# Optimization experiments

Hardware: AMD Instinct MI355X
Metric: run time of the kernel (lower is better)

The kernel has to match this reference:

```python
import jax, jax.numpy as jnp
import numpy as np

B, T, F, E, H = 1024, 128, 32, 16, 20
EPS = 1e-3  # keras BatchNormalization default epsilon
D = T * F   # flatten dim; fc1 builds with units = T*F due to pre-build units mutation


def lstm_relu(x, Wk, Wr, b, return_seq):
    """Keras LSTM with activation='relu', recurrent_activation=sigmoid.
    Gate order i, f, c(g), o. x: [B,T,Fin]. Returns [B,T,H] or [B,H]."""
    Bn = x.shape[0]
    h0 = jnp.zeros((Bn, H), x.dtype)
    c0 = jnp.zeros((Bn, H), x.dtype)

    def step(carry, xt):
        h, c = carry
        z = xt @ Wk + h @ Wr + b                      # [B, 4H]
        i, f, g, o = jnp.split(z, 4, axis=-1)
        i = jax.nn.sigmoid(i)
        f = jax.nn.sigmoid(f)
        g = jax.nn.relu(g)
        o = jax.nn.sigmoid(o)
        c = f * c + i * g
        h = o * jax.nn.relu(c)
        return (h, c), h

    (hT, _), hs = jax.lax.scan(step, (h0, c0), jnp.swapaxes(x, 0, 1))
    return jnp.swapaxes(hs, 0, 1) if return_seq else hT


def setup_inputs():
    key = jax.random.key(0)
    ks = jax.random.split(key, 16)
    s = 0.1
    d = {}
    d["x"] = jax.random.normal(ks[0], (B, T, F), jnp.float32)
    # BatchNorm (inference: moving stats)
    d["bn_gamma"] = jnp.ones((F,), jnp.float32)
    d["bn_beta"] = jnp.zeros((F,), jnp.float32)
    d["bn_mean"] = jax.random.normal(ks[1], (F,), jnp.float32) * 0.1
    d["bn_var"] = jax.random.uniform(ks[2], (F,), jnp.float32, 0.5, 1.5)
    # Per-expert LSTM stacks (stacked over expert axis E)
    d["k1"] = jax.random.normal(ks[3], (E, F, 4 * H), jnp.float32) * s
    d["r1"] = jax.random.normal(ks[4], (E, H, 4 * H), jnp.float32) * s
    d["b1"] = jnp.zeros((E, 4 * H), jnp.float32)
    d["k2"] = jax.random.normal(ks[5], (E, H, 4 * H), jnp.float32) * s
    d["r2"] = jax.random.normal(ks[6], (E, H, 4 * H), jnp.float32) * s
    d["b2"] = jnp.zeros((E, 4 * H), jnp.float32)
    d["dw"] = jax.random.normal(ks[7], (E, H, 1), jnp.float32) * s
    d["db"] = jnp.zeros((E, 1), jnp.float32)
    # Gating path: flatten -> Dense(D, relu) -> Dense(E, softmax)
    d["fc1_w"] = jax.random.normal(ks[8], (D, D), jnp.float32) * 0.02
    d["fc1_b"] = jnp.zeros((D,), jnp.float32)
    d["gate_w"] = jax.random.normal(ks[9], (D, E), jnp.float32) * 0.02
    d["gate_b"] = jnp.zeros((E,), jnp.float32)
    return d


def reference(x, bn_gamma, bn_beta, bn_mean, bn_var,
              k1, r1, b1, k2, r2, b2, dw, db,
              fc1_w, fc1_b, gate_w, gate_b):
    # BatchNorm (inference) over last axis
    xn = (x - bn_mean) * jax.lax.rsqrt(bn_var + EPS) * bn_gamma + bn_beta

    def run_expert(k1e, r1e, b1e, k2e, r2e, b2e, dwe, dbe):
        h1 = lstm_relu(xn, k1e, r1e, b1e, return_seq=True)    # [B,T,H]
        h2 = lstm_relu(h1, k2e, r2e, b2e, return_seq=False)   # [B,H]
        return h2 @ dwe + dbe                                  # [B,1]

    expert_outputs = jax.vmap(run_expert)(k1, r1, b1, k2, r2, b2, dw, db)  # [E,B,1]

    flat = x.reshape(x.shape[0], -1)                    # [B, T*F] (raw inputs, not normed)
    g = jax.nn.relu(flat @ fc1_w + fc1_b)               # [B, D]
    w = jax.nn.softmax(g @ gate_w + gate_b, axis=-1)    # [B, E]

    # stack(axis=1) -> [B,E,1]; weights expand_dims(axis=2) -> [B,E,1]; sum over E
    out = jnp.sum(jnp.transpose(expert_outputs, (1, 0, 2)) * w[:, :, None], axis=1)  # [B,1]
    return out
```

## Files before the change

kernel.cpp:

```cpp
#include <hip/hip_runtime.h>
#include <math.h>

#define Bsz 1024
#define Tt  128
#define Ff  32
#define Ee  16
#define Hh  20
#define Dd  4096
#define EPSc 1e-3f
#define LOG2E 1.4426950408889634f

#define PWE 7520

typedef __attribute__((ext_vector_type(8))) short bf16x8;
typedef __attribute__((ext_vector_type(4))) float f32x4;
typedef __attribute__((ext_vector_type(4))) unsigned int u32x4;

#define MFMA16(a,b,c) __builtin_amdgcn_mfma_f32_16x16x32_bf16(a, b, c, 0, 0, 0)

__device__ __forceinline__ float sig2(float z) {
    return __builtin_amdgcn_rcpf(1.0f + __builtin_amdgcn_exp2f(-z));
}
__device__ __forceinline__ unsigned short bf16_rne(float f) {
    unsigned u = __float_as_uint(f);
    u += 0x7FFFu + ((u >> 16) & 1u);
    return (unsigned short)(u >> 16);
}
__device__ __forceinline__ float bf16_to_f(unsigned short h) {
    return __uint_as_float(((unsigned)h) << 16);
}
__device__ __forceinline__ void cvt2(float f0, float f1, unsigned& hp, unsigned& lp) {
    asm("v_cvt_pk_bf16_f32 %0, %1, %2" : "=v"(hp) : "v"(f0), "v"(f1));
    float h0 = __uint_as_float(hp << 16);
    float h1 = __uint_as_float(hp & 0xFFFF0000u);
    asm("v_cvt_pk_bf16_f32 %0, %1, %2" : "=v"(lp) : "v"(f0 - h0), "v"(f1 - h1));
}

__global__ void xpack_kernel(const float* __restrict__ x,
                             const float* __restrict__ gamma, const float* __restrict__ beta,
                             const float* __restrict__ mean,  const float* __restrict__ var,
                             unsigned short* __restrict__ xph, unsigned short* __restrict__ xpl)
{
    __shared__ float sc[Ff], sh[Ff];
    int tid = threadIdx.x;
    if (tid < Ff) {
        float s = gamma[tid] * rsqrtf(var[tid] + EPSc);
        sc[tid] = s;
        sh[tid] = beta[tid] - mean[tid] * s;
    }
    __syncthreads();
    int idx = blockIdx.x * 256 + tid;
    int c   = idx >> 13;
    int rem = idx & 8191;
    int t   = rem >> 6;
    int l   = rem & 63;
    int q   = l >> 4, s = l & 15;
    const float* xr = x + ((size_t)(c * 16 + s) * Tt + t) * Ff + q * 8;
    float4 v0 = *(const float4*)xr;
    float4 v1 = *(const float4*)(xr + 4);
    float xv[8] = {v0.x, v0.y, v0.z, v0.w, v1.x, v1.y, v1.z, v1.w};
    bf16x8 hv, lv;
#pragma unroll
    for (int j = 0; j < 8; ++j) {
        int f = q * 8 + j;
        float xn_ = xv[j] * sc[f] + sh[f];
        unsigned short hi = bf16_rne(xn_);
        hv[j] = (short)hi;
        lv[j] = (short)bf16_rne(xn_ - bf16_to_f(hi));
    }
    *(bf16x8*)(xph + (size_t)idx * 8) = hv;
    *(bf16x8*)(xpl + (size_t)idx * 8) = lv;
}

__global__ void repack2_kernel(const float* __restrict__ k1, const float* __restrict__ r1,
                               const float* __restrict__ b1, const float* __restrict__ k2,
                               const float* __restrict__ r2, const float* __restrict__ b2,
                               float* __restrict__ pw)
{
    int idx = blockIdx.x * blockDim.x + threadIdx.x;
    if (idx >= Ee * PWE) return;
    int e = idx / PWE;
    int o = idx % PWE;
    float v;
    int g;
    if (o < 7360) {
        int c = o % 80, u = c >> 2;
        g = c & 3;
        int co = g * 20 + u;
        if (o < 2560) {
            int kk = o / 80;
            v = k1[((size_t)e * Ff + kk) * 80 + co];
        } else if (o < 4160) {
            int kk = (o - 2560) / 80;
            v = r1[((size_t)e * Hh + kk) * 80 + co];
        } else if (o < 5760) {
            int kk = (o - 4160) / 80;
            v = k2[((size_t)e * Hh + kk) * 80 + co];
        } else {
            int kk = (o - 5760) / 80;
            v = r2[((size_t)e * Hh + kk) * 80 + co];
        }
    } else if (o < 7440) {
        int c = o - 7360, u = c >> 2;
        g = c & 3;
        v = b1[(size_t)e * 80 + g * 20 + u];
    } else {
        int c = o - 7440, u = c >> 2;
        g = c & 3;
        v = b2[(size_t)e * 80 + g * 20 + u];
    }
    if (g != 2) v *= LOG2E;
    pw[idx] = v;
}

__global__ __launch_bounds__(256, 2) void fused_kernel(
    const unsigned short* __restrict__ xph, const unsigned short* __restrict__ xpl,
    const float* __restrict__ pw, const float* __restrict__ dw, const float* __restrict__ db,
    float* __restrict__ eo,
    const float* __restrict__ x, const float* __restrict__ W,
    const float* __restrict__ bias, float* __restrict__ C)
{
    __shared__ __align__(16) char smem[43008];

    if (blockIdx.x < 256) {
        const int l = threadIdx.x & 63;
        const int q = l >> 4, s = l & 15;
        const int tile = (blockIdx.x << 2) + (threadIdx.x >> 6);
        const int e = tile >> 6;
        const int c = tile & 63;
        const int b0 = c * 16;

        const float* Wm = pw + (size_t)e * PWE;
        bf16x8 K1h[5], K1l[5], R1h[5], R1l[5], K2h[5], K2l[5], R2h[5], R2l[5];
#pragma unroll
        for (int n = 0; n < 5; ++n) {
#pragma unroll
            for (int j = 0; j < 8; ++j) {
                int k8 = q * 8 + j;
                int uk = 4 * j + q;
                int cc = n * 16 + s;
                float wv_;
                unsigned short hi; float hf;
                wv_ = Wm[k8 * 80 + cc];
                hi = bf16_rne(wv_); hf = bf16_to_f(hi);
                K1h[n][j] = (short)hi; K1l[n][j] = (short)bf16_rne(wv_ - hf);
                wv_ = (j < 5) ? Wm[2560 + uk * 80 + cc] : 0.f;
                hi = bf16_rne(wv_); hf = bf16_to_f(hi);
                R1h[n][j] = (short)hi; R1l[n][j] = (short)bf16_rne(wv_ - hf);
                wv_ = (j < 5) ? Wm[4160 + uk * 80 + cc] : 0.f;
                hi = bf16_rne(wv_); hf = bf16_to_f(hi);
                K2h[n][j] = (short)hi; K2l[n][j] = (short)bf16_rne(wv_ - hf);
                wv_ = (j < 5) ? Wm[5760 + uk * 80 + cc] : 0.f;
                hi = bf16_rne(wv_); hf = bf16_to_f(hi);
                R2h[n][j] = (short)hi; R2l[n][j] = (short)bf16_rne(wv_ - hf);
            }
        }
        f32x4 bf1[5], bf2[5];
        float dwr[5];
#pragma unroll
        for (int n = 0; n < 5; ++n) {
            bf1[n] = *(const f32x4*)&Wm[7360 + n * 16 + 4 * q];
            bf2[n] = *(const f32x4*)&Wm[7440 + n * 16 + 4 * q];
            dwr[n] = dw[e * Hh + 4 * n + q];
        }

        float c1[5] = {0, 0, 0, 0, 0}, c2[5] = {0, 0, 0, 0, 0};
        float h2reg[5] = {0, 0, 0, 0, 0};

        const bf16x8 z8 = {0, 0, 0, 0, 0, 0, 0, 0};
        bf16x8 H1a = z8, H1b = z8, H2a = z8, H2b = z8;

        const unsigned short* xbh = xph + (size_t)c * 65536 + l * 8;
        const unsigned short* xbl = xpl + (size_t)c * 65536 + l * 8;
        bf16x8 xch = *(const bf16x8*)xbh;
        bf16x8 xcl = *(const bf16x8*)xbl;

#pragma unroll 1
        for (int t = 0; t < Tt; ++t) {
            bf16x8 xnh = xch, xnl = xcl;
            if (t < Tt - 1) {
                xnh = *(const bf16x8*)(xbh + (t + 1) * 512);
                xnl = *(const bf16x8*)(xbl + (t + 1) * 512);
            }

            f32x4 a1[5];
#pragma unroll
            for (int n = 0; n < 5; ++n) {
                f32x4 acc = bf1[n];
                acc = MFMA16(K1h[n], xch, acc);
                acc = MFMA16(K1l[n], xch, acc);
                acc = MFMA16(K1h[n], xcl, acc);
                acc = MFMA16(R1h[n], H1a, acc);
                acc = MFMA16(R1l[n], H1a, acc);
                acc = MFMA16(R1h[n], H1b, acc);
                a1[n] = acc;
            }
            {
                float hv[5];
#pragma unroll
                for (int n = 0; n < 5; ++n) {
                    float iv = sig2(a1[n][0]);
                    float fv = sig2(a1[n][1]);
                    float gv = fmaxf(a1[n][2], 0.f);
                    float ov = sig2(a1[n][3]);
                    c1[n] = fv * c1[n] + iv * gv;
                    hv[n] = ov * fmaxf(c1[n], 0.f);
                }
                unsigned h0, h1, h2, l0, l1, l2;
                cvt2(hv[0], hv[1], h0, l0);
                cvt2(hv[2], hv[3], h1, l1);
                cvt2(hv[4], 0.f,   h2, l2);
                u32x4 uh = {h0, h1, h2, 0u}, ul = {l0, l1, l2, 0u};
                H1a = __builtin_bit_cast(bf16x8, uh);
                H1b = __builtin_bit_cast(bf16x8, ul);
            }

            f32x4 a2[5];
#pragma unroll
            for (int n = 0; n < 5; ++n) {
                f32x4 acc = bf2[n];
                acc = MFMA16(R2h[n], H2a, acc);
                acc = MFMA16(R2l[n], H2a, acc);
                acc = MFMA16(R2h[n], H2b, acc);
                acc = MFMA16(K2h[n], H1a, acc);
                acc = MFMA16(K2l[n], H1a, acc);
                acc = MFMA16(K2h[n], H1b, acc);
                a2[n] = acc;
            }
            {
                float hv[5];
#pragma unroll
                for (int n = 0; n < 5; ++n) {
                    float iv = sig2(a2[n][0]);
                    float fv = sig2(a2[n][1]);
                    float gv = fmaxf(a2[n][2], 0.f);
                    float ov = sig2(a2[n][3]);
                    c2[n] = fv * c2[n] + iv * gv;
                    float h = ov * fmaxf(c2[n], 0.f);
                    h2reg[n] = h;
                    hv[n] = h;
                }
                unsigned h0, h1, h2, l0, l1, l2;
                cvt2(hv[0], hv[1], h0, l0);
                cvt2(hv[2], hv[3], h1, l1);
                cvt2(hv[4], 0.f,   h2, l2);
                u32x4 uh = {h0, h1, h2, 0u}, ul = {l0, l1, l2, 0u};
                H2a = __builtin_bit_cast(bf16x8, uh);
                H2b = __builtin_bit_cast(bf16x8, ul);
            }

            xch = xnh; xcl = xnl;
        }

        float p = 0.f;
#pragma unroll
        for (int n = 0; n < 5; ++n) p += h2reg[n] * dwr[n];
        p += __shfl_xor(p, 16);
        p += __shfl_xor(p, 32);
        if (q == 0) eo[(size_t)e * Bsz + b0 + s] = db[e] + p;

    } else {
        const int tid = threadIdx.x;
        const int wv = tid >> 6, l = tid & 63, q = l >> 4, s = l & 15;
        const int id = blockIdx.x & 255;
        const int n0 = (id & 31) * 128, m0 = (id >> 5) * 128;
        const int wr = (wv & 1) * 64, wc = (wv >> 1) * 64;

        const int wn = tid & 127, wkq = tid >> 7;
        const int wrot = (wn >> 3) & 3;
        const int ws0 = ((wkq * 2) + wrot) & 3;
        const int ws1 = ((wkq * 2 + 1) + wrot) & 3;

        const float* WG = W + (size_t)(wkq * 16) * Dd + n0 + wn;
        const float* Arow = x + (size_t)(m0 + wr + s) * Dd + q * 8;

        unsigned short* lds = (unsigned short*)smem;

        f32x4 acc[4][4];
#pragma unroll
        for (int mt = 0; mt < 4; ++mt)
#pragma unroll
            for (int nt = 0; nt < 4; ++nt) acc[mt][nt] = (f32x4){0.f, 0.f, 0.f, 0.f};

        float wfp[16];
        float4 afc[8];

        {
            float w0[16];
#pragma unroll
            for (int i = 0; i < 16; ++i) w0[i] = WG[(size_t)i * Dd];
            uint4 h0, l0, h1, l1;
            cvt2(w0[0],  w0[1],  h0.x, l0.x); cvt2(w0[2],  w0[3],  h0.y, l0.y);
            cvt2(w0[4],  w0[5],  h0.z, l0.z); cvt2(w0[6],  w0[7],  h0.w, l0.w);
            cvt2(w0[8],  w0[9],  h1.x, l1.x); cvt2(w0[10], w0[11], h1.y, l1.y);
            cvt2(w0[12], w0[13], h1.z, l1.z); cvt2(w0[14], w0[15], h1.w, l1.w);
            *(uint4*)&lds[wn * 40 + ws0 * 8]          = h0;
            *(uint4*)&lds[5120 + wn * 40 + ws0 * 8]   = l0;
            *(uint4*)&lds[wn * 40 + ws1 * 8]          = h1;
            *(uint4*)&lds[5120 + wn * 40 + ws1 * 8]   = l1;
#pragma unroll
            for (int i = 0; i < 16; ++i) wfp[i] = WG[(size_t)(32 + i) * Dd];
#pragma unroll
            for (int mt = 0; mt < 4; ++mt) {
                afc[mt * 2]     = *(const float4*)(Arow + (size_t)mt * 16 * Dd);
                afc[mt * 2 + 1] = *(const float4*)(Arow + (size_t)mt * 16 * Dd + 4);
            }
            __syncthreads();
        }

#pragma unroll 1
        for (int it = 0; it < 128; ++it) {
            const int k0 = it * 32;
            unsigned short* cb = lds + (it & 1) * 10240;
            unsigned short* sb = lds + ((it & 1) ^ 1) * 10240;

            if (it < 127) {
                uint4 h0, l0, h1, l1;
                cvt2(wfp[0],  wfp[1],  h0.x, l0.x); cvt2(wfp[2],  wfp[3],  h0.y, l0.y);
                cvt2(wfp[4],  wfp[5],  h0.z, l0.z); cvt2(wfp[6],  wfp[7],  h0.w, l0.w);
                cvt2(wfp[8],  wfp[9],  h1.x, l1.x); cvt2(wfp[10], wfp[11], h1.y, l1.y);
                cvt2(wfp[12], wfp[13], h1.z, l1.z); cvt2(wfp[14], wfp[15], h1.w, l1.w);
                *(uint4*)&sb[wn * 40 + ws0 * 8]        = h0;
                *(uint4*)&sb[5120 + wn * 40 + ws0 * 8] = l0;
                *(uint4*)&sb[wn * 40 + ws1 * 8]        = h1;
                *(uint4*)&sb[5120 + wn * 40 + ws1 * 8] = l1;
            }

            {
                const int kW = (it + 2 < 128) ? k0 + 64 : k0;
#pragma unroll
                for (int i = 0; i < 16; ++i) wfp[i] = WG[(size_t)(kW + i) * Dd];
            }

            bf16x8 Wfh[4], Wfl[4];
#pragma unroll
            for (int nt = 0; nt < 4; ++nt) {
                const int row = wc + nt * 16 + s;
                const int ps = (q + ((row >> 3) & 3)) & 3;
                Wfh[nt] = *(bf16x8*)&cb[row * 40 + ps * 8];
                Wfl[nt] = *(bf16x8*)&cb[5120 + row * 40 + ps * 8];
            }

            bf16x8 Afh[4], Afl[4];
#pragma unroll
            for (int mt = 0; mt < 4; ++mt) {
                uint4 uh, ul;
                cvt2(afc[mt * 2].x,     afc[mt * 2].y,     uh.x, ul.x);
                cvt2(afc[mt * 2].z,     afc[mt * 2].w,     uh.y, ul.y);
                cvt2(afc[mt * 2 + 1].x, afc[mt * 2 + 1].y, uh.z, ul.z);
                cvt2(afc[mt * 2 + 1].z, afc[mt * 2 + 1].w, uh.w, ul.w);
                Afh[mt] = __builtin_bit_cast(bf16x8, uh);
                Afl[mt] = __builtin_bit_cast(bf16x8, ul);
            }
            {
                const int kA = (it + 1 < 128) ? k0 + 32 : k0;
#pragma unroll
                for (int mt = 0; mt < 4; ++mt) {
                    afc[mt * 2]     = *(const float4*)(Arow + (size_t)mt * 16 * Dd + kA);
                    afc[mt * 2 + 1] = *(const float4*)(Arow + (size_t)mt * 16 * Dd + kA + 4);
                }
            }

#pragma unroll
            for (int mt = 0; mt < 4; ++mt)
#pragma unroll
                for (int nt = 0; nt < 4; ++nt) {
                    f32x4 a = acc[mt][nt];
                    a = MFMA16(Afl[mt], Wfh[nt], a);
                    a = MFMA16(Afh[mt], Wfl[nt], a);
                    a = MFMA16(Afh[mt], Wfh[nt], a);
                    acc[mt][nt] = a;
                }

            __syncthreads();
        }

#pragma unroll
        for (int nt = 0; nt < 4; ++nt) {
            float bv = bias[n0 + wc + nt * 16 + s];
#pragma unroll
            for (int mt = 0; mt < 4; ++mt)
#pragma unroll
                for (int r = 0; r < 4; ++r) {
                    int m = m0 + wr + mt * 16 + q * 4 + r;
                    C[(size_t)m * Dd + n0 + wc + nt * 16 + s] = fmaxf(acc[mt][nt][r] + bv, 0.f);
                }
        }
    }
}

__global__ __launch_bounds__(256) void gate_kernel(const float* __restrict__ g,
                                                   const float* __restrict__ gw,
                                                   const float* __restrict__ gb,
                                                   const float* __restrict__ eo,
                                                   float* __restrict__ out)
{
    int b = blockIdx.x;
    int tid = threadIdx.x;
    int lane = tid & 63;
    int wv = tid >> 6;

    float acc[16];
#pragma unroll
    for (int j = 0; j < 16; ++j) acc[j] = 0.f;

    const float* grow = g + (size_t)b * Dd;
#pragma unroll
    for (int it = 0; it < Dd / 256; ++it) {
        int d = tid + it * 256;
        float gv = grow[d];
        const float4* wr = (const float4*)(gw + (size_t)d * 16);
        float4 w0 = wr[0], w1 = wr[1], w2 = wr[2], w3 = wr[3];
        acc[0] += gv * w0.x;  acc[1] += gv * w0.y;  acc[2] += gv * w0.z;  acc[3] += gv * w0.w;
        acc[4] += gv * w1.x;  acc[5] += gv * w1.y;  acc[6] += gv * w1.z;  acc[7] += gv * w1.w;
        acc[8] += gv * w2.x;  acc[9] += gv * w2.y;  acc[10] += gv * w2.z; acc[11] += gv * w2.w;
        acc[12] += gv * w3.x; acc[13] += gv * w3.y; acc[14] += gv * w3.z; acc[15] += gv * w3.w;
    }

    __shared__ float red[64];
    __shared__ float logits[16];
#pragma unroll
    for (int j = 0; j < 16; ++j) {
        float v = acc[j];
#pragma unroll
        for (int m = 32; m >= 1; m >>= 1) v += __shfl_xor(v, m);
        if (lane == 0) red[wv * 16 + j] = v;
    }
    __syncthreads();
    if (tid < 16) {
        logits[tid] = gb[tid] + red[tid] + red[16 + tid] + red[32 + tid] + red[48 + tid];
    }
    __syncthreads();
    if (tid == 0) {
        float m = logits[0];
#pragma unroll
        for (int j = 1; j < 16; ++j) m = fmaxf(m, logits[j]);
        float ex[16], ssum = 0.f;
#pragma unroll
        for (int j = 0; j < 16; ++j) { ex[j] = __expf(logits[j] - m); ssum += ex[j]; }
        float inv = 1.f / ssum;
        float o = 0.f;
#pragma unroll
        for (int j = 0; j < 16; ++j) o += ex[j] * inv * eo[(size_t)j * Bsz + b];
        out[b] = o;
    }
}

extern "C" void kernel_launch(void* const* d_in, const int* in_sizes, int n_in,
                              void* d_out, int out_size, void* d_ws, size_t ws_size,
                              hipStream_t stream)
{
    const float* x     = (const float*)d_in[0];
    const float* gamma = (const float*)d_in[1];
    const float* beta  = (const float*)d_in[2];
    const float* mean  = (const float*)d_in[3];
    const float* var   = (const float*)d_in[4];
    const float* k1    = (const float*)d_in[5];
    const float* r1    = (const float*)d_in[6];
    const float* b1    = (const float*)d_in[7];
    const float* k2    = (const float*)d_in[8];
    const float* r2    = (const float*)d_in[9];
    const float* b2    = (const float*)d_in[10];
    const float* dw    = (const float*)d_in[11];
    const float* db    = (const float*)d_in[12];
    const float* fc1w  = (const float*)d_in[13];
    const float* fc1b  = (const float*)d_in[14];
    const float* gw    = (const float*)d_in[15];
    const float* gb    = (const float*)d_in[16];
    float* out = (float*)d_out;

    float* g = (float*)d_ws;
    unsigned short* xph = (unsigned short*)(g + (size_t)Bsz * Dd);
    unsigned short* xpl = xph + (size_t)Bsz * Dd / 2 * 2;
    float* pw  = (float*)(xpl + (size_t)4194304);
    float* eo  = pw + (size_t)Ee * PWE;

    xpack_kernel<<<2048, 256, 0, stream>>>(x, gamma, beta, mean, var, xph, xpl);
    repack2_kernel<<<(Ee * PWE + 255) / 256, 256, 0, stream>>>(k1, r1, b1, k2, r2, b2, pw);
    fused_kernel<<<512, 256, 0, stream>>>(xph, xpl, pw, dw, db, eo, x, fc1w, fc1b, g);
    gate_kernel<<<Bsz, 256, 0, stream>>>(g, gw, gb, eo, out);
}
```

Before: 467.5 us.

## Halve GEMM tile rows, raise occupancy, batch gate kernel over four rows

The fc1 GEMM part of the fused kernel now uses 64x128 tiles instead of 128x128, giving 512 GEMM blocks (768 total) and a launch bound of 3 blocks per CU. The aim is to spread the GEMM across more CUs alongside the long-running LSTM blocks and to cut registers per thread. The LDS swizzle rotation is also adjusted. The gate kernel now handles four batch rows per block so each gate-weight load is reused four times. The trade-offs are more W traffic per output and possible register spills in the LSTM path under the tighter launch bound.

```diff
diff --git a/kernel.cpp b/kernel.cpp
--- a/kernel.cpp
+++ b/kernel.cpp
@@ -113,7 +113,7 @@
     pw[idx] = v;
 }
 
-__global__ __launch_bounds__(256, 2) void fused_kernel(
+__global__ __launch_bounds__(256, 3) void fused_kernel(
     const unsigned short* __restrict__ xph, const unsigned short* __restrict__ xpl,
     const float* __restrict__ pw, const float* __restrict__ dw, const float* __restrict__ db,
     float* __restrict__ eo,
@@ -262,12 +262,12 @@
     } else {
         const int tid = threadIdx.x;
         const int wv = tid >> 6, l = tid & 63, q = l >> 4, s = l & 15;
-        const int id = blockIdx.x & 255;
-        const int n0 = (id & 31) * 128, m0 = (id >> 5) * 128;
-        const int wr = (wv & 1) * 64, wc = (wv >> 1) * 64;
+        const int id = blockIdx.x - 256;
+        const int n0 = (id & 31) * 128, m0 = (id >> 5) * 64;
+        const int wr = (wv & 1) * 32, wc = (wv >> 1) * 64;
 
         const int wn = tid & 127, wkq = tid >> 7;
-        const int wrot = (wn >> 3) & 3;
+        const int wrot = ((wn >> 3) + (wn >> 5)) & 3;
         const int ws0 = ((wkq * 2) + wrot) & 3;
         const int ws1 = ((wkq * 2 + 1) + wrot) & 3;
 
@@ -276,14 +276,14 @@
 
         unsigned short* lds = (unsigned short*)smem;
 
-        f32x4 acc[4][4];
-#pragma unroll
-        for (int mt = 0; mt < 4; ++mt)
+        f32x4 acc[2][4];
+#pragma unroll
+        for (int mt = 0; mt < 2; ++mt)
 #pragma unroll
             for (int nt = 0; nt < 4; ++nt) acc[mt][nt] = (f32x4){0.f, 0.f, 0.f, 0.f};
 
         float wfp[16];
-        float4 afc[8];
+        float4 afc[4];
 
         {
             float w0[16];
@@ -301,7 +301,7 @@
 #pragma unroll
             for (int i = 0; i < 16; ++i) wfp[i] = WG[(size_t)(32 + i) * Dd];
 #pragma unroll
-            for (int mt = 0; mt < 4; ++mt) {
+            for (int mt = 0; mt < 2; ++mt) {
                 afc[mt * 2]     = *(const float4*)(Arow + (size_t)mt * 16 * Dd);
                 afc[mt * 2 + 1] = *(const float4*)(Arow + (size_t)mt * 16 * Dd + 4);
             }
@@ -336,14 +336,14 @@
 #pragma unroll
             for (int nt = 0; nt < 4; ++nt) {
                 const int row = wc + nt * 16 + s;
-                const int ps = (q + ((row >> 3) & 3)) & 3;
+                const int ps = (q + ((row >> 3) + (row >> 5))) & 3;
                 Wfh[nt] = *(bf16x8*)&cb[row * 40 + ps * 8];
                 Wfl[nt] = *(bf16x8*)&cb[5120 + row * 40 + ps * 8];
             }
 
-            bf16x8 Afh[4], Afl[4];
-#pragma unroll
-            for (int mt = 0; mt < 4; ++mt) {
+            bf16x8 Afh[2], Afl[2];
+#pragma unroll
+            for (int mt = 0; mt < 2; ++mt) {
                 uint4 uh, ul;
                 cvt2(afc[mt * 2].x,     afc[mt * 2].y,     uh.x, ul.x);
                 cvt2(afc[mt * 2].z,     afc[mt * 2].w,     uh.y, ul.y);
@@ -355,14 +355,14 @@
             {
                 const int kA = (it + 1 < 128) ? k0 + 32 : k0;
 #pragma unroll
-                for (int mt = 0; mt < 4; ++mt) {
+                for (int mt = 0; mt < 2; ++mt) {
                     afc[mt * 2]     = *(const float4*)(Arow + (size_t)mt * 16 * Dd + kA);
                     afc[mt * 2 + 1] = *(const float4*)(Arow + (size_t)mt * 16 * Dd + kA + 4);
                 }
             }
 
 #pragma unroll
-            for (int mt = 0; mt < 4; ++mt)
+            for (int mt = 0; mt < 2; ++mt)
 #pragma unroll
                 for (int nt = 0; nt < 4; ++nt) {
                     f32x4 a = acc[mt][nt];
@@ -379,7 +379,7 @@
         for (int nt = 0; nt < 4; ++nt) {
             float bv = bias[n0 + wc + nt * 16 + s];
 #pragma unroll
-            for (int mt = 0; mt < 4; ++mt)
+            for (int mt = 0; mt < 2; ++mt)
 #pragma unroll
                 for (int r = 0; r < 4; ++r) {
                     int m = m0 + wr + mt * 16 + q * 4 + r;
@@ -395,49 +395,65 @@
                                                    const float* __restrict__ eo,
                                                    float* __restrict__ out)
 {
-    int b = blockIdx.x;
+    int b0 = blockIdx.x * 4;
     int tid = threadIdx.x;
     int lane = tid & 63;
     int wv = tid >> 6;
 
-    float acc[16];
-#pragma unroll
-    for (int j = 0; j < 16; ++j) acc[j] = 0.f;
-
-    const float* grow = g + (size_t)b * Dd;
+    float acc[4][16];
+#pragma unroll
+    for (int bb = 0; bb < 4; ++bb)
+#pragma unroll
+        for (int j = 0; j < 16; ++j) acc[bb][j] = 0.f;
+
+    const float* g0 = g + (size_t)b0 * Dd;
 #pragma unroll
     for (int it = 0; it < Dd / 256; ++it) {
         int d = tid + it * 256;
-        float gv = grow[d];
-        const float4* wr = (const float4*)(gw + (size_t)d * 16);
-        float4 w0 = wr[0], w1 = wr[1], w2 = wr[2], w3 = wr[3];
-        acc[0] += gv * w0.x;  acc[1] += gv * w0.y;  acc[2] += gv * w0.z;  acc[3] += gv * w0.w;
-        acc[4] += gv * w1.x;  acc[5] += gv * w1.y;  acc[6] += gv * w1.z;  acc[7] += gv * w1.w;
-        acc[8] += gv * w2.x;  acc[9] += gv * w2.y;  acc[10] += gv * w2.z; acc[11] += gv * w2.w;
-        acc[12] += gv * w3.x; acc[13] += gv * w3.y; acc[14] += gv * w3.z; acc[15] += gv * w3.w;
-    }
-
-    __shared__ float red[64];
-    __shared__ float logits[16];
-#pragma unroll
-    for (int j = 0; j < 16; ++j) {
-        float v = acc[j];
-#pragma unroll
-        for (int m = 32; m >= 1; m >>= 1) v += __shfl_xor(v, m);
-        if (lane == 0) red[wv * 16 + j] = v;
-    }
+        const float4* wr_ = (const float4*)(gw + (size_t)d * 16);
+        float4 w0 = wr_[0], w1 = wr_[1], w2 = wr_[2], w3 = wr_[3];
+        float gv[4];
+#pragma unroll
+        for (int bb = 0; bb < 4; ++bb) gv[bb] = g0[(size_t)bb * Dd + d];
+#pragma unroll
+        for (int bb = 0; bb < 4; ++bb) {
+            float v = gv[bb];
+            acc[bb][0]  += v * w0.x;  acc[bb][1]  += v * w0.y;
+            acc[bb][2]  += v * w0.z;  acc[bb][3]  += v * w0.w;
+            acc[bb][4]  += v * w1.x;  acc[bb][5]  += v * w1.y;
+            acc[bb][6]  += v * w1.z;  acc[bb][7]  += v * w1.w;
+            acc[bb][8]  += v * w2.x;  acc[bb][9]  += v * w2.y;
+            acc[bb][10] += v * w2.z;  acc[bb][11] += v * w2.w;
+            acc[bb][12] += v * w3.x;  acc[bb][13] += v * w3.y;
+            acc[bb][14] += v * w3.z;  acc[bb][15] += v * w3.w;
+        }
+    }
+
+    __shared__ float red[4][4][16];
+    __shared__ float logits[4][16];
+#pragma unroll
+    for (int bb = 0; bb < 4; ++bb)
+#pragma unroll
+        for (int j = 0; j < 16; ++j) {
+            float v = acc[bb][j];
+#pragma unroll
+            for (int m = 32; m >= 1; m >>= 1) v += __shfl_xor(v, m);
+            if (lane == 0) red[wv][bb][j] = v;
+        }
     __syncthreads();
-    if (tid < 16) {
-        logits[tid] = gb[tid] + red[tid] + red[16 + tid] + red[32 + tid] + red[48 + tid];
+    if (tid < 64) {
+        int bb = tid >> 4, j = tid & 15;
+        logits[bb][j] = gb[j] + red[0][bb][j] + red[1][bb][j] + red[2][bb][j] + red[3][bb][j];
     }
     __syncthreads();
-    if (tid == 0) {
-        float m = logits[0];
-#pragma unroll
-        for (int j = 1; j < 16; ++j) m = fmaxf(m, logits[j]);
+    if (tid < 4) {
+        int b = b0 + tid;
+        float m = logits[tid][0];
+#pragma unroll
+        for (int j = 1; j < 16; ++j) m = fmaxf(m, logits[tid][j]);
         float ex[16], ssum = 0.f;
 #pragma unroll
-        for (int j = 0; j < 16; ++j) { ex[j] = __expf(logits[j] - m); ssum += ex[j]; }
+        for (int j = 0; j < 16; ++j) { ex[j] = __expf(logits[tid][j] - m); ssum += ex[j]; }
         float inv = 1.f / ssum;
         float o = 0.f;
 #pragma unroll
@@ -477,6 +493,6 @@
 
     xpack_kernel<<<2048, 256, 0, stream>>>(x, gamma, beta, mean, var, xph, xpl);
     repack2_kernel<<<(Ee * PWE + 255) / 256, 256, 0, stream>>>(k1, r1, b1, k2, r2, b2, pw);
-    fused_kernel<<<512, 256, 0, stream>>>(xph, xpl, pw, dw, db, eo, x, fc1w, fc1b, g);
-    gate_kernel<<<Bsz, 256, 0, stream>>>(g, gw, gb, eo, out);
-}
+    fused_kernel<<<768, 256, 0, stream>>>(xph, xpl, pw, dw, db, eo, x, fc1w, fc1b, g);
+    gate_kernel<<<Bsz / 4, 256, 0, stream>>>(g, gw, gb, eo, out);
+}
```

Result: slower. 888.0 us (+90.0%).
